# Optimization experiments

Measured on AMD Instinct MI355X. Metric: run time of the kernel, lower is better.

The kernel has to match this reference:

```python
import jax, jax.numpy as jnp
import numpy as np

V, E, H, D = 32000, 512, 512, 3          # vocab, embed_dim, hidden_dim, max_depth
PD = max(H // 4, 16)                      # policy depth-embed dim = 128
DEPTH_EMBED_SCALE = 0.01
SIB_SCALE = 1.0 / np.sqrt(H)              # sibling_scale default 1/sqrt(hidden_dim)
GREEDY_THRESHOLD = 0.5
PROB_MIN, PROB_MAX = 1e-7, 1.0 - 1e-7


def _ln(x, g, b, eps=1e-5):
    m = x.mean(-1, keepdims=True)
    v = jnp.var(x, axis=-1, keepdims=True)
    return (x - m) * jax.lax.rsqrt(v + eps) * g + b


def setup_inputs() -> dict:
    key = jax.random.key(0)
    ks = jax.random.split(key, 12)
    def n(k, shape, s=0.02):
        return jax.random.normal(k, shape, jnp.float32) * s
    return {
        "token_ids": jax.random.randint(ks[0], (4096,), 0, V),
        "emb": n(ks[1], (V, E)),                      # embedding table
        "proj_w": n(ks[2], (H, E), 0.04), "proj_b": jnp.zeros(H, jnp.float32),
        "cf_w": n(ks[3], (2 * H, H), 0.04), "cf_b": jnp.zeros(2 * H, jnp.float32),
        "in_g": jnp.ones(H, jnp.float32), "in_b": jnp.zeros(H, jnp.float32),   # policy input LayerNorm
        "pde": n(ks[4], (D + 1, PD), 0.01),           # policy depth embedding
        "f1w": n(ks[5], (H // 2, H + PD), 0.04), "f1b": jnp.zeros(H // 2, jnp.float32),
        "n1g": jnp.ones(H // 2, jnp.float32), "n1b": jnp.zeros(H // 2, jnp.float32),
        "f2w": n(ks[6], (H // 4, H // 2), 0.06), "f2b": jnp.zeros(H // 4, jnp.float32),
        "n2g": jnp.ones(H // 4, jnp.float32), "n2b": jnp.zeros(H // 4, jnp.float32),
        "pow_w": n(ks[7], (1, H // 4), 0.01), "pow_b": jnp.zeros(1, jnp.float32),
        "sib": n(ks[8], (2, H)),                      # sibling embeddings (left/right)
        "dep": n(ks[9], (D + 1, H), 0.01),            # tree depth embeddings
        "out_w": n(ks[10], (V, H), 0.04), "out_b": jnp.zeros(V, jnp.float32),
    }


def _forward(token_ids, emb, proj_w, proj_b, cf_w, cf_b, in_g, in_b, pde,
             f1w, f1b, n1g, n1b, f2w, f2b, n2g, n2b, pow_w, pow_b,
             sib, dep, out_w, out_b):
    # h0: project token embeddings to hidden space. [N, H]
    h0 = emb[token_ids] @ proj_w.T + proj_b
    nodes = h0[None]                      # level-0 nodes: [1, N, H]
    agg_sum = h0                          # running sum over all tree nodes
    agg_cnt = jnp.float32(1.0)
    alive = jnp.float32(1.0)              # cumulative greedy-expand mask
    for level in range(D):
        # growth policy on the level-mean hidden (+ scaled depth embedding)
        lh = nodes.mean(0) + DEPTH_EMBED_SCALE * dep[level]          # [N, H]
        hn = _ln(lh, in_g, in_b)
        de = jnp.broadcast_to(pde[min(level, D)], (hn.shape[0], PD))
        x = jnp.concatenate([hn, de], axis=-1)
        x = jax.nn.relu(_ln(x @ f1w.T + f1b, n1g, n1b))
        x = jax.nn.relu(_ln(x @ f2w.T + f2b, n2g, n2b))
        p = jax.nn.sigmoid((x @ pow_w.T + pow_b)[..., 0])             # [N]
        p_mean = jnp.clip(p, PROB_MIN, PROB_MAX).mean()
        alive = alive * (p_mean >= GREEDY_THRESHOLD).astype(jnp.float32)
        # binary child expansion: child_fc then chunk into left/right + sibling embeds
        cf = jnp.einsum('mnh,kh->mnk', nodes, cf_w) + cf_b            # [M, N, 2H]
        left = cf[..., :H] + SIB_SCALE * sib[0]
        right = cf[..., H:] + SIB_SCALE * sib[1]
        nodes = jnp.concatenate([left, right], axis=0)                # [2M, N, H]
        agg_sum = agg_sum + alive * nodes.sum(0)
        agg_cnt = agg_cnt + alive * jnp.float32(nodes.shape[0])
    pooled = agg_sum / jnp.maximum(agg_cnt, 1e-8)                     # mean pooling
    return pooled @ out_w.T + out_b                                   # [N, V]


def reference(token_ids, emb, proj_w, proj_b, cf_w, cf_b, in_g, in_b, pde,
              f1w, f1b, n1g, n1b, f2w, f2b, n2g, n2b, pow_w, pow_b,
              sib, dep, out_w, out_b):
    return _forward(token_ids, emb, proj_w, proj_b, cf_w, cf_b, in_g, in_b, pde,
                    f1w, f1b, n1g, n1b, f2w, f2b, n2g, n2b, pow_w, pow_b,
                    sib, dep, out_w, out_b)
```

## Files before the change

kernel.cpp:

```cpp
#include <hip/hip_runtime.h>

typedef unsigned short u16;
using bf16x8 = __attribute__((ext_vector_type(8))) short;
using f32x4  = __attribute__((ext_vector_type(4))) float;

#define SIB_SCALE_F 0.04419417382415922f

__device__ __forceinline__ u16 f2b(float f) {
  unsigned u = __builtin_bit_cast(unsigned, f);
  return (u16)((u + 0x7FFFu + ((u >> 16) & 1u)) >> 16);
}

__device__ __forceinline__ float wred(float v) {
  #pragma unroll
  for (int m = 1; m < 64; m <<= 1) v += __shfl_xor(v, m);
  return v;
}

__device__ __forceinline__ void gload16(const void* g, void* l) {
  __builtin_amdgcn_global_load_lds(
      (const __attribute__((address_space(1))) unsigned int*)g,
      (__attribute__((address_space(3))) unsigned int*)l, 16, 0, 0);
}

__global__ __launch_bounds__(512, 2) void gemmP(
    const u16* __restrict__ A, const u16* __restrict__ B,
    const float* __restrict__ bias,
    float* __restrict__ C, int M, int N, int K, int MT)
{
  __shared__ u16 lds[65536];
  const int t = threadIdx.x, w = t >> 6, lane = t & 63;
  const int wm = w >> 2, wn = w & 3;
  const int r16 = lane & 15, ks = lane >> 4;

  const int bn = blockIdx.y * 256;
  const int mg = blockIdx.x;
  const int NT = K >> 6;

  auto stageH = [&](const u16* __restrict__ G, int grow0, int kt, int half, int opBase) {
    const int k0 = kt << 6;
    u16* dst = lds + opBase + ((kt & 1) << 14) + (half << 13);
    #pragma unroll
    for (int j = 0; j < 2; ++j) {
      const int r = half * 128 + j * 64 + w * 8 + (lane >> 3);
      const int s = (lane & 7) ^ (r & 7);
      gload16(G + (size_t)(grow0 + r) * K + k0 + s * 8,
              dst + j * 4096 + w * 512);
    }
  };

  for (int mt = 0; mt < MT; ++mt) {
    const int bm = (mg * MT + mt) * 256;

    f32x4 acc[8][4];
    #pragma unroll
    for (int m = 0; m < 8; ++m)
      #pragma unroll
      for (int n = 0; n < 4; ++n) {
        f32x4 z = {0.f, 0.f, 0.f, 0.f};
        acc[m][n] = z;
      }

    __builtin_amdgcn_sched_barrier(0);
    stageH(A, bm, 0, 0, 0);
    stageH(A, bm, 0, 1, 0);
    stageH(B, bn, 0, 0, 32768);
    stageH(B, bn, 0, 1, 32768);
    __builtin_amdgcn_sched_barrier(0);
    stageH(B, bn, 1, 0, 32768);
    stageH(B, bn, 1, 1, 32768);
    asm volatile("s_waitcnt vmcnt(4)" ::: "memory");
    __builtin_amdgcn_sched_barrier(0);
    __builtin_amdgcn_s_barrier();

    for (int kt = 0; kt < NT; ++kt) {
      const u16* Ab = lds + ((kt & 1) << 14);
      const u16* Bb = lds + 32768 + ((kt & 1) << 14);
      bf16x8 bfr[4][2];

      #pragma unroll
      for (int p = 0; p < 4; ++p) {
        bf16x8 af2[2][2];
        #pragma unroll
        for (int i = 0; i < 2; ++i) {
          const int row = wm * 128 + (2 * p + i) * 16 + r16;
          af2[i][0] = *(const bf16x8*)(Ab + row * 64 + ((ks ^ (row & 7)) << 3));
          af2[i][1] = *(const bf16x8*)(Ab + row * 64 + (((4 + ks) ^ (row & 7)) << 3));
        }
        if (p == 0) {
          #pragma unroll
          for (int n = 0; n < 4; ++n) {
            const int row = wn * 64 + n * 16 + r16;
            bfr[n][0] = *(const bf16x8*)(Bb + row * 64 + ((ks ^ (row & 7)) << 3));
            bfr[n][1] = *(const bf16x8*)(Bb + row * 64 + (((4 + ks) ^ (row & 7)) << 3));
          }
        }
        if (p == 0 && kt + 1 < NT) stageH(A, bm, kt + 1, 0, 0);
        if (p == 1 && kt + 1 < NT) stageH(A, bm, kt + 1, 1, 0);
        if (p == 2 && kt + 2 < NT) stageH(B, bn, kt + 2, 0, 32768);
        if (p == 3) {
          if (kt + 2 < NT) {
            stageH(B, bn, kt + 2, 1, 32768);
            asm volatile("s_waitcnt vmcnt(4)" ::: "memory");
          } else {
            asm volatile("s_waitcnt vmcnt(0)" ::: "memory");
          }
          __builtin_amdgcn_sched_barrier(0);
        }
        __builtin_amdgcn_s_barrier();
        asm volatile("s_waitcnt lgkmcnt(0)" ::: "memory");
        __builtin_amdgcn_sched_barrier(0);
        __builtin_amdgcn_s_setprio(1);
        #pragma unroll
        for (int i = 0; i < 2; ++i)
          #pragma unroll
          for (int n = 0; n < 4; ++n) {
            acc[2 * p + i][n] = __builtin_amdgcn_mfma_f32_16x16x32_bf16(
                bfr[n][0], af2[i][0], acc[2 * p + i][n], 0, 0, 0);
            acc[2 * p + i][n] = __builtin_amdgcn_mfma_f32_16x16x32_bf16(
                bfr[n][1], af2[i][1], acc[2 * p + i][n], 0, 0, 0);
          }
        __builtin_amdgcn_s_setprio(0);
        __builtin_amdgcn_s_barrier();
      }
    }

    #pragma unroll
    for (int m = 0; m < 8; ++m) {
      const int grow = bm + wm * 128 + m * 16 + r16;
      float* Crow = C + (size_t)grow * N;
      #pragma unroll
      for (int n = 0; n < 4; ++n) {
        const int gcol = bn + wn * 64 + n * 16 + ks * 4;
        const float4 bv = *(const float4*)(bias + gcol);
        float4 o;
        o.x = acc[m][n][0] + bv.x;
        o.y = acc[m][n][1] + bv.y;
        o.z = acc[m][n][2] + bv.z;
        o.w = acc[m][n][3] + bv.w;
        *(float4*)(Crow + gcol) = o;
      }
    }
  }
}

template <bool GATHER, bool POOL>
__global__ __launch_bounds__(256) void gemm_bf16_bt(
    const float* __restrict__ Afp, const int* __restrict__ tok,
    const u16* __restrict__ A, const u16* __restrict__ B,
    const float* __restrict__ bias, int blvl, float bscale,
    float* __restrict__ C, u16* __restrict__ Cb,
    const float* __restrict__ h0f, const float* __restrict__ S1f,
    const float* __restrict__ S2f, const float* __restrict__ psum,
    u16* __restrict__ P,
    int M, int N, int K)
{
  __shared__ u16 ldsA[128 * 32];
  __shared__ u16 ldsB[128 * 32];
  const int t = threadIdx.x;
  const int w = t >> 6;
  const int lane = t & 63;
  const int wr = w >> 1, wc = w & 1;

  const int nb = gridDim.x * gridDim.y;
  const int lid = blockIdx.y * gridDim.x + blockIdx.x;
  const int chunk = nb >> 3;
  const int nlid = (lid & 7) * chunk + (lid >> 3);
  const int bx = nlid % gridDim.x, by = nlid / gridDim.x;

  const int bm = bx * 128, bn = by * 128;
  const int r16 = lane & 15, ks = lane >> 4;
  const int srow = t >> 2, sslot = t & 3;

  f32x4 acc[4][4];
  #pragma unroll
  for (int m = 0; m < 4; ++m)
    #pragma unroll
    for (int n = 0; n < 4; ++n) {
      f32x4 z = {0.f, 0.f, 0.f, 0.f};
      acc[m][n] = z;
    }

  for (int k0 = 0; k0 < K; k0 += 32) {
    if (k0) __syncthreads();
    #pragma unroll
    for (int i = 0; i < 2; ++i) {
      const int row = srow + i * 64;
      const int sl = sslot ^ ((row >> 1) & 3);
      if constexpr (GATHER) {
        const float* src = Afp + (size_t)tok[bm + row] * 512 + k0 + sl * 8;
        const float4 a0 = *(const float4*)src;
        const float4 a1 = *(const float4*)(src + 4);
        bf16x8 v;
        v[0] = (short)f2b(a0.x); v[1] = (short)f2b(a0.y);
        v[2] = (short)f2b(a0.z); v[3] = (short)f2b(a0.w);
        v[4] = (short)f2b(a1.x); v[5] = (short)f2b(a1.y);
        v[6] = (short)f2b(a1.z); v[7] = (short)f2b(a1.w);
        *(bf16x8*)(ldsA + i * 2048 + w * 512 + lane * 8) = v;
      } else {
        gload16(A + (size_t)(bm + row) * K + k0 + sl * 8,
                ldsA + (i * 2048 + w * 512));
      }
      gload16(B + (size_t)(bn + row) * K + k0 + sl * 8,
              ldsB + (i * 2048 + w * 512));
    }
    __syncthreads();

    bf16x8 af[4], bfr[4];
    #pragma unroll
    for (int m = 0; m < 4; ++m) {
      const int row = wr * 64 + m * 16 + r16;
      af[m] = *(const bf16x8*)(ldsA + row * 32 + ((ks ^ ((row >> 1) & 3)) << 3));
    }
    #pragma unroll
    for (int n = 0; n < 4; ++n) {
      const int row = wc * 64 + n * 16 + r16;
      bfr[n] = *(const bf16x8*)(ldsB + row * 32 + ((ks ^ ((row >> 1) & 3)) << 3));
    }
    #pragma unroll
    for (int m = 0; m < 4; ++m)
      #pragma unroll
      for (int n = 0; n < 4; ++n)
        acc[m][n] = __builtin_amdgcn_mfma_f32_16x16x32_bf16(bfr[n], af[m], acc[m][n], 0, 0, 0);
  }

  const float* be = bias + (size_t)(bm >> 12) * blvl;

  float a0 = 0.f, a1 = 0.f, a2 = 0.f, inv = 0.f;
  if constexpr (POOL) {
    a0 = (psum[0] * (1.f / 4096.f) >= 0.5f) ? 1.f : 0.f;
    a1 = a0 * ((psum[1] * (1.f / 4096.f) >= 0.5f) ? 1.f : 0.f);
    a2 = a1 * ((psum[2] * (1.f / 4096.f) >= 0.5f) ? 1.f : 0.f);
    const float cnt = 1.f + a0 * 2.f + a1 * 4.f + a2 * 8.f;
    inv = 1.f / fmaxf(cnt, 1e-8f);
  }

  #pragma unroll
  for (int m = 0; m < 4; ++m) {
    const int grow = bm + wr * 64 + m * 16 + r16;
    #pragma unroll
    for (int n = 0; n < 4; ++n) {
      const int gcol = bn + wc * 64 + n * 16 + ks * 4;
      const float4 bv = *(const float4*)(be + gcol);
      float4 o;
      o.x = acc[m][n][0] + bv.x * bscale;
      o.y = acc[m][n][1] + bv.y * bscale;
      o.z = acc[m][n][2] + bv.z * bscale;
      o.w = acc[m][n][3] + bv.w * bscale;
      const size_t idx = (size_t)grow * N + gcol;
      if constexpr (POOL) {
        const float4 h = *(const float4*)(h0f + idx);
        const float4 s1 = *(const float4*)(S1f + idx);
        const float4 s2 = *(const float4*)(S2f + idx);
        ushort4 ob;
        ob.x = f2b((h.x + a0 * s1.x + a1 * s2.x + a2 * o.x) * inv);
        ob.y = f2b((h.y + a0 * s1.y + a1 * s2.y + a2 * o.y) * inv);
        ob.z = f2b((h.z + a0 * s1.z + a1 * s2.z + a2 * o.z) * inv);
        ob.w = f2b((h.w + a0 * s1.w + a1 * s2.w + a2 * o.w) * inv);
        *(ushort4*)(P + idx) = ob;
      } else {
        *(float4*)(C + idx) = o;
        if (Cb) {
          ushort4 ob = { f2b(o.x), f2b(o.y), f2b(o.z), f2b(o.w) };
          *(ushort4*)(Cb + idx) = ob;
        }
      }
    }
  }
}

__global__ __launch_bounds__(256) void prep_misc(
    const float* __restrict__ cf_w, const float* __restrict__ cf_b,
    const float* __restrict__ sib, const float* __restrict__ proj_w,
    const float* __restrict__ f1w, const float* __restrict__ f1b,
    const float* __restrict__ f2w, const float* __restrict__ pde,
    const float* __restrict__ out_w,
    u16* __restrict__ wsum_b, u16* __restrict__ projw_b,
    u16* __restrict__ f1w512b, u16* __restrict__ f2wb,
    float* __restrict__ cvec, float* __restrict__ psum,
    float* __restrict__ y1bias, u16* __restrict__ outw_b)
{
  const int b = blockIdx.x, t = threadIdx.x;
  if (b >= 676) {
    const int idx = (b - 676) * 256 + t;
    const float4 v = ((const float4*)out_w)[idx];
    ushort4 o = { f2b(v.x), f2b(v.y), f2b(v.z), f2b(v.w) };
    ((ushort4*)outw_b)[idx] = o;
  } else if (b < 256) {
    const int idx = b * 256 + t;
    const float4 a = ((const float4*)cf_w)[idx];
    const float4 c = ((const float4*)(cf_w + 262144))[idx];
    ushort4 o = { f2b(a.x + c.x), f2b(a.y + c.y), f2b(a.z + c.z), f2b(a.w + c.w) };
    ((ushort4*)wsum_b)[idx] = o;
  } else if (b < 512) {
    const int idx = (b - 256) * 256 + t;
    const float4 v = ((const float4*)proj_w)[idx];
    ushort4 o = { f2b(v.x), f2b(v.y), f2b(v.z), f2b(v.w) };
    ((ushort4*)projw_b)[idx] = o;
  } else if (b < 640) {
    const int fi = (b - 512) * 256 + t;
    const int row = fi >> 7, c4 = fi & 127;
    const float4 v = *(const float4*)(f1w + (size_t)row * 640 + c4 * 4);
    ushort4 o = { f2b(v.x), f2b(v.y), f2b(v.z), f2b(v.w) };
    ((ushort4*)f1w512b)[row * 128 + c4] = o;
  } else if (b < 672) {
    const int idx = (b - 640) * 256 + t;
    const float4 v = ((const float4*)f2w)[idx];
    ushort4 o = { f2b(v.x), f2b(v.y), f2b(v.z), f2b(v.w) };
    ((ushort4*)f2wb)[idx] = o;
  } else if (b < 675) {
    const int l = b - 672, j = t;
    const float* wrow = f1w + (size_t)j * 640 + 512;
    const float* p = pde + l * 128;
    float s = f1b[j];
    #pragma unroll 4
    for (int k = 0; k < 128; ++k) s += wrow[k] * p[k];
    y1bias[l * 256 + j] = s;
  } else {
    cvec[t]       = cf_b[t]       + cf_b[512 + t] + SIB_SCALE_F * (sib[t]       + sib[512 + t]);
    cvec[256 + t] = cf_b[256 + t] + cf_b[768 + t] + SIB_SCALE_F * (sib[256 + t] + sib[768 + t]);
    if (t < 3) psum[t] = 0.f;
  }
}

__global__ __launch_bounds__(256) void mean_ln_concat_b(
    const float* __restrict__ S0, const float* __restrict__ S1,
    const float* __restrict__ S2,
    const float* __restrict__ dep,
    const float* __restrict__ g, const float* __restrict__ b,
    u16* __restrict__ X)
{
  const int wid = threadIdx.x >> 6, lane = threadIdx.x & 63;
  const int gr = blockIdx.x * 4 + wid;
  const int l = gr >> 12, n = gr & 4095;
  const float* Sr = (l == 0 ? S0 : l == 1 ? S1 : S2) + (size_t)n * 512;
  const float invM = (l == 0 ? 1.f : l == 1 ? 0.5f : 0.25f);
  const float* depl = dep + 512 * l;
  const int c0 = lane * 8;
  float x[8];
  float s = 0.f, sq = 0.f;
  #pragma unroll
  for (int i = 0; i < 8; ++i) {
    const float v = Sr[c0 + i] * invM + 0.01f * depl[c0 + i];
    x[i] = v; s += v; sq += v * v;
  }
  s = wred(s); sq = wred(sq);
  const float mean = s * (1.f / 512.f);
  const float var = sq * (1.f / 512.f) - mean * mean;
  const float rs = rsqrtf(var + 1e-5f);
  ushort4 o0, o1;
  o0.x = f2b((x[0] - mean) * rs * g[c0 + 0] + b[c0 + 0]);
  o0.y = f2b((x[1] - mean) * rs * g[c0 + 1] + b[c0 + 1]);
  o0.z = f2b((x[2] - mean) * rs * g[c0 + 2] + b[c0 + 2]);
  o0.w = f2b((x[3] - mean) * rs * g[c0 + 3] + b[c0 + 3]);
  o1.x = f2b((x[4] - mean) * rs * g[c0 + 4] + b[c0 + 4]);
  o1.y = f2b((x[5] - mean) * rs * g[c0 + 5] + b[c0 + 5]);
  o1.z = f2b((x[6] - mean) * rs * g[c0 + 6] + b[c0 + 6]);
  o1.w = f2b((x[7] - mean) * rs * g[c0 + 7] + b[c0 + 7]);
  ushort4* Xr = (ushort4*)(X + (size_t)gr * 512);
  Xr[lane * 2]     = o0;
  Xr[lane * 2 + 1] = o1;
}

__global__ __launch_bounds__(256) void ln_relu_b256(
    const float* __restrict__ X, const float* __restrict__ g,
    const float* __restrict__ b, u16* __restrict__ O)
{
  const int wid = threadIdx.x >> 6, lane = threadIdx.x & 63;
  const int n = blockIdx.x * 4 + wid;
  const float* Xr = X + (size_t)n * 256;
  float x[4];
  float s = 0.f, sq = 0.f;
  #pragma unroll
  for (int i = 0; i < 4; ++i) {
    x[i] = Xr[lane * 4 + i]; s += x[i]; sq += x[i] * x[i];
  }
  s = wred(s); sq = wred(sq);
  const float mean = s * (1.f / 256.f);
  const float var = sq * (1.f / 256.f) - mean * mean;
  const float rs = rsqrtf(var + 1e-5f);
  ushort4 o;
  o.x = f2b(fmaxf((x[0] - mean) * rs * g[lane * 4 + 0] + b[lane * 4 + 0], 0.f));
  o.y = f2b(fmaxf((x[1] - mean) * rs * g[lane * 4 + 1] + b[lane * 4 + 1], 0.f));
  o.z = f2b(fmaxf((x[2] - mean) * rs * g[lane * 4 + 2] + b[lane * 4 + 2], 0.f));
  o.w = f2b(fmaxf((x[3] - mean) * rs * g[lane * 4 + 3] + b[lane * 4 + 3], 0.f));
  ((ushort4*)(O + (size_t)n * 256))[lane] = o;
}

__global__ __launch_bounds__(256) void ln_policy128(
    const float* __restrict__ Y2, const float* __restrict__ g,
    const float* __restrict__ b, const float* __restrict__ pw,
    const float* __restrict__ pb, float* __restrict__ psum)
{
  __shared__ float part[4];
  const int wid = threadIdx.x >> 6, lane = threadIdx.x & 63;
  const int gr = blockIdx.x * 4 + wid;
  const float* Xr = Y2 + (size_t)gr * 128;
  float x[2];
  float s = 0.f, sq = 0.f;
  #pragma unroll
  for (int i = 0; i < 2; ++i) {
    x[i] = Xr[lane * 2 + i]; s += x[i]; sq += x[i] * x[i];
  }
  s = wred(s); sq = wred(sq);
  const float mean = s * (1.f / 128.f);
  const float var = sq * (1.f / 128.f) - mean * mean;
  const float rs = rsqrtf(var + 1e-5f);
  float z = 0.f;
  #pragma unroll
  for (int i = 0; i < 2; ++i) {
    const int c = lane * 2 + i;
    const float v = fmaxf((x[i] - mean) * rs * g[c] + b[c], 0.f);
    z += v * pw[c];
  }
  z = wred(z);
  if (lane == 0) {
    const float p = 1.f / (1.f + expf(-(z + pb[0])));
    part[wid] = fminf(fmaxf(p, 1e-7f), 1.f - 1e-7f);
  }
  __syncthreads();
  if (threadIdx.x == 0)
    atomicAdd(psum + (gr >> 12), part[0] + part[1] + part[2] + part[3]);
}

extern "C" void kernel_launch(void* const* d_in, const int* in_sizes, int n_in,
                              void* d_out, int out_size, void* d_ws, size_t ws_size,
                              hipStream_t stream) {
  const int*   tok    = (const int*)  d_in[0];
  const float* emb    = (const float*)d_in[1];
  const float* proj_w = (const float*)d_in[2];
  const float* proj_b = (const float*)d_in[3];
  const float* cf_w   = (const float*)d_in[4];
  const float* cf_b   = (const float*)d_in[5];
  const float* in_g   = (const float*)d_in[6];
  const float* in_b   = (const float*)d_in[7];
  const float* pde    = (const float*)d_in[8];
  const float* f1w    = (const float*)d_in[9];
  const float* f1b    = (const float*)d_in[10];
  const float* n1g    = (const float*)d_in[11];
  const float* n1b    = (const float*)d_in[12];
  const float* f2w    = (const float*)d_in[13];
  const float* f2bias = (const float*)d_in[14];
  const float* n2g    = (const float*)d_in[15];
  const float* n2b    = (const float*)d_in[16];
  const float* pow_w  = (const float*)d_in[17];
  const float* pow_b  = (const float*)d_in[18];
  const float* sib    = (const float*)d_in[19];
  const float* dep    = (const float*)d_in[20];
  const float* out_w  = (const float*)d_in[21];
  const float* out_b  = (const float*)d_in[22];
  float* out = (float*)d_out;

  char* ws = (char*)d_ws;
  size_t off = 0;
  auto alloc = [&](size_t bytes) -> void* {
    void* p = ws + off;
    off += (bytes + 255) & ~(size_t)255;
    return p;
  };
  u16*   outw_b  = (u16*)  alloc((size_t)32000 * 512 * 2);
  u16*   projw_b = (u16*)  alloc((size_t)512 * 512 * 2);
  u16*   wsum_b  = (u16*)  alloc((size_t)512 * 512 * 2);
  u16*   f1w512b = (u16*)  alloc((size_t)256 * 512 * 2);
  u16*   f2wb    = (u16*)  alloc((size_t)128 * 256 * 2);
  float* h0f     = (float*)alloc((size_t)4096 * 512 * 4);
  u16*   h0b     = (u16*)  alloc((size_t)4096 * 512 * 2);
  float* S1f     = (float*)alloc((size_t)4096 * 512 * 4);
  u16*   S1b     = (u16*)  alloc((size_t)4096 * 512 * 2);
  float* S2f     = (float*)alloc((size_t)4096 * 512 * 4);
  u16*   S2b     = (u16*)  alloc((size_t)4096 * 512 * 2);
  u16*   X       = (u16*)  alloc((size_t)12288 * 512 * 2);
  float* Y1      = (float*)alloc((size_t)12288 * 256 * 4);
  u16*   Y1b     = (u16*)  alloc((size_t)12288 * 256 * 2);
  float* Y2      = (float*)alloc((size_t)12288 * 128 * 4);
  float* y1bias  = (float*)alloc(3 * 256 * 4);
  float* cvec    = (float*)alloc(512 * 4);
  float* psum    = (float*)alloc(256);
  u16*   poolb   = (u16*)  alloc((size_t)4096 * 512 * 2);

  prep_misc<<<16676, 256, 0, stream>>>(cf_w, cf_b, sib, proj_w, f1w, f1b, f2w,
                                       pde, out_w,
                                       wsum_b, projw_b, f1w512b, f2wb,
                                       cvec, psum, y1bias, outw_b);

  gemm_bf16_bt<true, false><<<dim3(32, 4), 256, 0, stream>>>(
      emb, tok, nullptr, projw_b, proj_b, 0, 1.f, h0f, h0b,
      nullptr, nullptr, nullptr, nullptr, nullptr, 4096, 512, 512);
  gemm_bf16_bt<false, false><<<dim3(32, 4), 256, 0, stream>>>(
      nullptr, nullptr, h0b, wsum_b, cvec, 0, 1.f, S1f, S1b,
      nullptr, nullptr, nullptr, nullptr, nullptr, 4096, 512, 512);
  gemm_bf16_bt<false, false><<<dim3(32, 4), 256, 0, stream>>>(
      nullptr, nullptr, S1b, wsum_b, cvec, 0, 2.f, S2f, S2b,
      nullptr, nullptr, nullptr, nullptr, nullptr, 4096, 512, 512);

  mean_ln_concat_b<<<3072, 256, 0, stream>>>(h0f, S1f, S2f, dep, in_g, in_b, X);
  gemm_bf16_bt<false, false><<<dim3(96, 2), 256, 0, stream>>>(
      nullptr, nullptr, X, f1w512b, y1bias, 256, 1.f, Y1, nullptr,
      nullptr, nullptr, nullptr, nullptr, nullptr, 12288, 256, 512);
  ln_relu_b256<<<3072, 256, 0, stream>>>(Y1, n1g, n1b, Y1b);
  gemm_bf16_bt<false, false><<<dim3(96, 1), 256, 0, stream>>>(
      nullptr, nullptr, Y1b, f2wb, f2bias, 0, 1.f, Y2, nullptr,
      nullptr, nullptr, nullptr, nullptr, nullptr, 12288, 128, 256);
  ln_policy128<<<3072, 256, 0, stream>>>(Y2, n2g, n2b, pow_w, pow_b, psum);

  gemm_bf16_bt<false, true><<<dim3(32, 4), 256, 0, stream>>>(
      nullptr, nullptr, S2b, wsum_b, cvec, 0, 4.f, nullptr, nullptr,
      h0f, S1f, S2f, psum, poolb, 4096, 512, 512);

  gemmP<<<dim3(2, 125), 512, 0, stream>>>(poolb, outw_b, out_b,
                                          out, 4096, 32000, 512, 8);
}
```

Baseline: 409.9 us.

## Restructure output GEMM to overlap epilogue stores with next tile's mainloop

The final vocab-projection GEMM changes from 256x256 tiles with K-step 64 to 128x256 tiles with K-step 32, which shrinks LDS from 128KB to 48KB. It keeps a second accumulator set so that the previous M-tile's results are written, one fragment per K step, while the next tile's MFMAs run. The idea is to hide the fp32 output store traffic behind compute and give a continuous load pipeline across tiles. In exchange it doubles accumulator registers (pacc), takes smaller K steps with more barriers per FLOP, and reuses less of the B tile per load.

```diff
diff --git a/kernel.cpp b/kernel.cpp
--- a/kernel.cpp
+++ b/kernel.cpp
@@ -23,123 +23,145 @@
       (__attribute__((address_space(3))) unsigned int*)l, 16, 0, 0);
 }
 
-__global__ __launch_bounds__(512, 2) void gemmP(
+__global__ __launch_bounds__(512, 2) void gemmQ(
     const u16* __restrict__ A, const u16* __restrict__ B,
     const float* __restrict__ bias,
     float* __restrict__ C, int M, int N, int K, int MT)
 {
-  __shared__ u16 lds[65536];
+  __shared__ u16 lds[24576];
   const int t = threadIdx.x, w = t >> 6, lane = t & 63;
   const int wm = w >> 2, wn = w & 3;
   const int r16 = lane & 15, ks = lane >> 4;
-
   const int bn = blockIdx.y * 256;
   const int mg = blockIdx.x;
-  const int NT = K >> 6;
-
-  auto stageH = [&](const u16* __restrict__ G, int grow0, int kt, int half, int opBase) {
-    const int k0 = kt << 6;
-    u16* dst = lds + opBase + ((kt & 1) << 14) + (half << 13);
+  const int NT = 16;
+  const int T = MT * NT;
+
+  auto stageT = [&](int g2) {
+    const int kt2 = g2 & 15;
+    const int bm2 = (mg * MT + (g2 >> 4)) * 128;
+    const int k0 = kt2 << 5;
+    const int b = g2 & 1;
+    {
+      const int row = t >> 2;
+      const int sl = (t & 3) ^ ((row >> 1) & 3);
+      gload16(A + (size_t)(bm2 + row) * K + k0 + sl * 8,
+              lds + b * 4096 + w * 512);
+    }
     #pragma unroll
     for (int j = 0; j < 2; ++j) {
-      const int r = half * 128 + j * 64 + w * 8 + (lane >> 3);
-      const int s = (lane & 7) ^ (r & 7);
-      gload16(G + (size_t)(grow0 + r) * K + k0 + s * 8,
-              dst + j * 4096 + w * 512);
+      const int row = j * 128 + (t >> 2);
+      const int sl = (t & 3) ^ ((row >> 1) & 3);
+      gload16(B + (size_t)(bn + row) * K + k0 + sl * 8,
+              lds + 8192 + b * 8192 + j * 4096 + w * 512);
     }
   };
 
-  for (int mt = 0; mt < MT; ++mt) {
-    const int bm = (mg * MT + mt) * 256;
-
-    f32x4 acc[8][4];
-    #pragma unroll
-    for (int m = 0; m < 8; ++m)
+  float4 biasv[4];
+  #pragma unroll
+  for (int n = 0; n < 4; ++n)
+    biasv[n] = *(const float4*)(bias + bn + wn * 64 + n * 16 + ks * 4);
+
+  f32x4 acc[4][4], pacc[4][4];
+  #pragma unroll
+  for (int m = 0; m < 4; ++m)
+    #pragma unroll
+    for (int n = 0; n < 4; ++n) {
+      f32x4 z = {0.f, 0.f, 0.f, 0.f};
+      acc[m][n] = z; pacc[m][n] = z;
+    }
+  int bmPrev = 0;
+
+  stageT(0); stageT(1);
+  asm volatile("s_waitcnt vmcnt(3)" ::: "memory");
+  __builtin_amdgcn_sched_barrier(0);
+  __builtin_amdgcn_s_barrier();
+
+  for (int gt = 0; gt < MT; ++gt) {
+    const int hasStore = (gt > 0);
+    #pragma unroll
+    for (int kt = 0; kt < 16; ++kt) {
+      const int g = gt * 16 + kt;
+      const int b = kt & 1;
+      const u16* Ab = lds + b * 4096;
+      const u16* Bb = lds + 8192 + b * 8192;
+
+      bf16x8 af[4], bf[4];
+      #pragma unroll
+      for (int m = 0; m < 4; ++m) {
+        const int row = wm * 64 + m * 16 + r16;
+        af[m] = *(const bf16x8*)(Ab + row * 32 + ((ks ^ ((row >> 1) & 3)) << 3));
+      }
       #pragma unroll
       for (int n = 0; n < 4; ++n) {
-        f32x4 z = {0.f, 0.f, 0.f, 0.f};
-        acc[m][n] = z;
-      }
-
-    __builtin_amdgcn_sched_barrier(0);
-    stageH(A, bm, 0, 0, 0);
-    stageH(A, bm, 0, 1, 0);
-    stageH(B, bn, 0, 0, 32768);
-    stageH(B, bn, 0, 1, 32768);
-    __builtin_amdgcn_sched_barrier(0);
-    stageH(B, bn, 1, 0, 32768);
-    stageH(B, bn, 1, 1, 32768);
-    asm volatile("s_waitcnt vmcnt(4)" ::: "memory");
-    __builtin_amdgcn_sched_barrier(0);
-    __builtin_amdgcn_s_barrier();
-
-    for (int kt = 0; kt < NT; ++kt) {
-      const u16* Ab = lds + ((kt & 1) << 14);
-      const u16* Bb = lds + 32768 + ((kt & 1) << 14);
-      bf16x8 bfr[4][2];
-
+        const int row = wn * 64 + n * 16 + r16;
+        bf[n] = *(const bf16x8*)(Bb + row * 32 + ((ks ^ ((row >> 1) & 3)) << 3));
+      }
+      asm volatile("s_waitcnt lgkmcnt(0)" ::: "memory");
+      __builtin_amdgcn_sched_barrier(0);
+      __builtin_amdgcn_s_barrier();
+
+      if (hasStore) {
+        constexpr int sm = 0;
+        (void)sm;
+        const int m = kt >> 2, n = kt & 3;
+        const int grow = bmPrev + wm * 64 + m * 16 + r16;
+        const int gcol = bn + wn * 64 + n * 16 + ks * 4;
+        float4 o;
+        o.x = pacc[kt >> 2][kt & 3][0] + biasv[kt & 3].x;
+        o.y = pacc[kt >> 2][kt & 3][1] + biasv[kt & 3].y;
+        o.z = pacc[kt >> 2][kt & 3][2] + biasv[kt & 3].z;
+        o.w = pacc[kt >> 2][kt & 3][3] + biasv[kt & 3].w;
+        *(float4*)(C + (size_t)grow * N + gcol) = o;
+        (void)m; (void)n;
+      }
+      const bool doStage = (g + 2 < T);
+      if (doStage) stageT(g + 2);
+
+      if (doStage) {
+        if (hasStore) asm volatile("s_waitcnt vmcnt(4)" ::: "memory");
+        else          asm volatile("s_waitcnt vmcnt(3)" ::: "memory");
+      } else {
+        asm volatile("s_waitcnt vmcnt(1)" ::: "memory");
+      }
+      __builtin_amdgcn_sched_barrier(0);
+      __builtin_amdgcn_s_barrier();
+
+      __builtin_amdgcn_s_setprio(1);
       #pragma unroll
-      for (int p = 0; p < 4; ++p) {
-        bf16x8 af2[2][2];
+      for (int m = 0; m < 4; ++m)
         #pragma unroll
-        for (int i = 0; i < 2; ++i) {
-          const int row = wm * 128 + (2 * p + i) * 16 + r16;
-          af2[i][0] = *(const bf16x8*)(Ab + row * 64 + ((ks ^ (row & 7)) << 3));
-          af2[i][1] = *(const bf16x8*)(Ab + row * 64 + (((4 + ks) ^ (row & 7)) << 3));
-        }
-        if (p == 0) {
+        for (int n = 0; n < 4; ++n)
+          acc[m][n] = __builtin_amdgcn_mfma_f32_16x16x32_bf16(bf[n], af[m], acc[m][n], 0, 0, 0);
+      __builtin_amdgcn_s_setprio(0);
+
+      if (kt == 15) {
+        bmPrev = (mg * MT + gt) * 128;
+        #pragma unroll
+        for (int m = 0; m < 4; ++m)
           #pragma unroll
           for (int n = 0; n < 4; ++n) {
-            const int row = wn * 64 + n * 16 + r16;
-            bfr[n][0] = *(const bf16x8*)(Bb + row * 64 + ((ks ^ (row & 7)) << 3));
-            bfr[n][1] = *(const bf16x8*)(Bb + row * 64 + (((4 + ks) ^ (row & 7)) << 3));
+            pacc[m][n] = acc[m][n];
+            f32x4 z = {0.f, 0.f, 0.f, 0.f};
+            acc[m][n] = z;
           }
-        }
-        if (p == 0 && kt + 1 < NT) stageH(A, bm, kt + 1, 0, 0);
-        if (p == 1 && kt + 1 < NT) stageH(A, bm, kt + 1, 1, 0);
-        if (p == 2 && kt + 2 < NT) stageH(B, bn, kt + 2, 0, 32768);
-        if (p == 3) {
-          if (kt + 2 < NT) {
-            stageH(B, bn, kt + 2, 1, 32768);
-            asm volatile("s_waitcnt vmcnt(4)" ::: "memory");
-          } else {
-            asm volatile("s_waitcnt vmcnt(0)" ::: "memory");
-          }
-          __builtin_amdgcn_sched_barrier(0);
-        }
-        __builtin_amdgcn_s_barrier();
-        asm volatile("s_waitcnt lgkmcnt(0)" ::: "memory");
-        __builtin_amdgcn_sched_barrier(0);
-        __builtin_amdgcn_s_setprio(1);
-        #pragma unroll
-        for (int i = 0; i < 2; ++i)
-          #pragma unroll
-          for (int n = 0; n < 4; ++n) {
-            acc[2 * p + i][n] = __builtin_amdgcn_mfma_f32_16x16x32_bf16(
-                bfr[n][0], af2[i][0], acc[2 * p + i][n], 0, 0, 0);
-            acc[2 * p + i][n] = __builtin_amdgcn_mfma_f32_16x16x32_bf16(
-                bfr[n][1], af2[i][1], acc[2 * p + i][n], 0, 0, 0);
-          }
-        __builtin_amdgcn_s_setprio(0);
-        __builtin_amdgcn_s_barrier();
-      }
-    }
-
-    #pragma unroll
-    for (int m = 0; m < 8; ++m) {
-      const int grow = bm + wm * 128 + m * 16 + r16;
-      float* Crow = C + (size_t)grow * N;
-      #pragma unroll
-      for (int n = 0; n < 4; ++n) {
-        const int gcol = bn + wn * 64 + n * 16 + ks * 4;
-        const float4 bv = *(const float4*)(bias + gcol);
-        float4 o;
-        o.x = acc[m][n][0] + bv.x;
-        o.y = acc[m][n][1] + bv.y;
-        o.z = acc[m][n][2] + bv.z;
-        o.w = acc[m][n][3] + bv.w;
-        *(float4*)(Crow + gcol) = o;
-      }
+      }
+    }
+  }
+
+  #pragma unroll
+  for (int m = 0; m < 4; ++m) {
+    const int grow = bmPrev + wm * 64 + m * 16 + r16;
+    float* Crow = C + (size_t)grow * N;
+    #pragma unroll
+    for (int n = 0; n < 4; ++n) {
+      const int gcol = bn + wn * 64 + n * 16 + ks * 4;
+      float4 o;
+      o.x = pacc[m][n][0] + biasv[n].x;
+      o.y = pacc[m][n][1] + biasv[n].y;
+      o.z = pacc[m][n][2] + biasv[n].z;
+      o.w = pacc[m][n][3] + biasv[n].w;
+      *(float4*)(Crow + gcol) = o;
     }
   }
 }
@@ -507,6 +529,6 @@
       nullptr, nullptr, S2b, wsum_b, cvec, 0, 4.f, nullptr, nullptr,
       h0f, S1f, S2f, psum, poolb, 4096, 512, 512);
 
-  gemmP<<<dim3(2, 125), 512, 0, stream>>>(poolb, outw_b, out_b,
-                                          out, 4096, 32000, 512, 8);
-}
+  gemmQ<<<dim3(2, 125), 512, 0, stream>>>(poolb, outw_b, out_b,
+                                          out, 4096, 32000, 512, 16);
+}
```

Measured after the change: 481.0 us. 17.4% more time.
